# Performance work log

Measured on AMD Instinct MI355X. Metric: run time of the kernel, lower is better.

Reference implementation:

```python
import jax, jax.numpy as jnp
import numpy as np

B, P, S, D = 16, 512, 1024, 1024
H_FULL, H_LIGHT = 16, 8


def _mha(q, k, v, w_in, b_in, w_out, b_out, nh):
    # PyTorch nn.MultiheadAttention (batch_first=True), dropout=0 (eval).
    d = q.shape[-1]
    hd = d // nh
    wq, wk, wv = jnp.split(w_in, 3, axis=0)
    bq, bk, bv = jnp.split(b_in, 3, axis=0)

    def proj(x, w, b):
        return (x @ w.T + b).reshape(x.shape[0], x.shape[1], nh, hd)

    qh = proj(q, wq, bq)  # [B,Lq,H,hd]
    kh = proj(k, wk, bk)  # [B,Lk,H,hd]
    vh = proj(v, wv, bv)
    scale = 1.0 / jnp.sqrt(jnp.asarray(hd, q.dtype))
    scores = jnp.einsum('bqhd,bkhd->bhqk', qh, kh) * scale
    attn = jax.nn.softmax(scores, axis=-1)
    o = jnp.einsum('bhqk,bkhd->bqhd', attn, vh).reshape(q.shape[0], q.shape[1], d)
    out = o @ w_out.T + b_out
    return out, attn.mean(axis=1)  # avg weights over heads (torch default)


def _ln(x, g, b, eps=1e-5):
    mu = x.mean(-1, keepdims=True)
    var = ((x - mu) ** 2).mean(-1, keepdims=True)
    return (x - mu) / jnp.sqrt(var + eps) * g + b


def setup_inputs() -> dict:
    key = jax.random.key(0)
    ks = jax.random.split(key, 16)
    w = 0.02
    inp = {
        'proto': jax.random.normal(ks[0], (B, P, D), jnp.float32),
        'img_features': jax.random.normal(ks[1], (B, S, D), jnp.float32),
        'cross_w_in': jax.random.normal(ks[2], (3 * D, D), jnp.float32) * w,
        'cross_b_in': jnp.zeros((3 * D,), jnp.float32),
        'cross_w_out': jax.random.normal(ks[3], (D, D), jnp.float32) * w,
        'cross_b_out': jnp.zeros((D,), jnp.float32),
        'self_w_in': jax.random.normal(ks[4], (3 * D, D), jnp.float32) * w,
        'self_b_in': jnp.zeros((3 * D,), jnp.float32),
        'self_w_out': jax.random.normal(ks[5], (D, D), jnp.float32) * w,
        'self_b_out': jnp.zeros((D,), jnp.float32),
        'light_w_in': jax.random.normal(ks[6], (3 * D, D), jnp.float32) * w,
        'light_b_in': jnp.zeros((3 * D,), jnp.float32),
        'light_w_out': jax.random.normal(ks[7], (D, D), jnp.float32) * w,
        'light_b_out': jnp.zeros((D,), jnp.float32),
        'norm1_g': jnp.ones((D,), jnp.float32), 'norm1_b': jnp.zeros((D,), jnp.float32),
        'norm2_g': jnp.ones((D,), jnp.float32), 'norm2_b': jnp.zeros((D,), jnp.float32),
        'norm3_g': jnp.ones((D,), jnp.float32), 'norm3_b': jnp.zeros((D,), jnp.float32),
        'gate_w1': jax.random.normal(ks[8], (D, 3 * D), jnp.float32) * w,
        'gate_b1': jnp.zeros((D,), jnp.float32),
        'gate_w2': jax.random.normal(ks[9], (3, D), jnp.float32) * w,
        'gate_b2': jnp.zeros((3,), jnp.float32),
    }
    return inp


def reference(proto, img_features,
              cross_w_in, cross_b_in, cross_w_out, cross_b_out,
              self_w_in, self_b_in, self_w_out, self_b_out,
              light_w_in, light_b_in, light_w_out, light_b_out,
              norm1_g, norm1_b, norm2_g, norm2_b, norm3_g, norm3_b,
              gate_w1, gate_b1, gate_w2, gate_b2):
    cross_raw, attn_w = _mha(proto, img_features, img_features,
                             cross_w_in, cross_b_in, cross_w_out, cross_b_out, H_FULL)
    cross_out = _ln(proto + cross_raw, norm1_g, norm1_b)
    self_raw, _ = _mha(cross_out, cross_out, cross_out,
                       self_w_in, self_b_in, self_w_out, self_b_out, H_FULL)
    self_out = _ln(cross_out + self_raw, norm2_g, norm2_b)
    light_raw, _ = _mha(self_out, self_out, self_out,
                        light_w_in, light_b_in, light_w_out, light_b_out, H_LIGHT)
    light_out = _ln(self_out + light_raw, norm3_g, norm3_b)
    gate_in = jnp.concatenate([cross_out, self_out, light_out], axis=-1)  # [B,P,3D]
    h = jax.nn.gelu(gate_in @ gate_w1.T + gate_b1, approximate=False)
    gate_w = jax.nn.softmax(h @ gate_w2.T + gate_b2, axis=-1)  # [B,P,3]
    updated = (gate_w[..., 0:1] * cross_out
               + gate_w[..., 1:2] * self_out
               + gate_w[..., 2:3] * light_out)
    return updated, attn_w
```

## Files before the change

### kernel.cpp

```cpp
#include <hip/hip_runtime.h>
#include <hip/hip_bf16.h>

typedef __hip_bfloat16 bf16;
typedef __attribute__((ext_vector_type(8))) short short8;
typedef __attribute__((ext_vector_type(4))) float f32x4;

#define BD 16
#define PD 512
#define SD 1024
#define DD 1024

#define GLDS16(gp, lp)                                              \
  __builtin_amdgcn_global_load_lds(                                 \
      (const __attribute__((address_space(1))) void*)(gp),          \
      (__attribute__((address_space(3))) void*)(lp), 16, 0, 0)

__global__ __launch_bounds__(256) void f2b(const float* __restrict__ in,
                                           bf16* __restrict__ out, int n)
{
  int i = (blockIdx.x * 256 + threadIdx.x) * 4;
  if (i < n) {
    float4 v = *(const float4*)(in + i);
    out[i + 0] = __float2bfloat16(v.x);
    out[i + 1] = __float2bfloat16(v.y);
    out[i + 2] = __float2bfloat16(v.z);
    out[i + 3] = __float2bfloat16(v.w);
  }
}

__global__ __launch_bounds__(256) void gemm_nt(
    const bf16* __restrict__ A, int lda,
    const bf16* __restrict__ W, int ldw,
    const float* __restrict__ bias,
    bf16* __restrict__ C, int ldc,
    int K, int gelu)
{
  __shared__ bf16 As[3][128 * 32];
  __shared__ bf16 Bs[3][64 * 32];

  const int t = threadIdx.x;
  const int lane = t & 63, wv = t >> 6;
  const int m0 = blockIdx.y * 128;
  const int n0 = blockIdx.x * 64;
  const int rl = lane & 15, qd = lane >> 4;

  f32x4 acc[4][2];
  for (int i = 0; i < 4; i++)
    for (int j = 0; j < 2; j++)
      acc[i][j] = (f32x4){0.f, 0.f, 0.f, 0.f};

  const int scol = ((t & 3) ^ ((t >> 2) & 3)) * 8;
  const bf16* Ag = A + (size_t)(m0 + (t >> 2)) * lda + scol;
  const bf16* Wg = W + (size_t)(n0 + (t >> 2)) * ldw + scol;
  const size_t a_half = (size_t)64 * lda;
  const int lo = wv * 512;

  const int mw = (wv >> 1) * 64, nw = (wv & 1) * 32;
  const int slo = rl & 3;

  const int nt = K >> 5;

#define STAGE(buf, k0)                               \
  do {                                               \
    GLDS16(Ag + (k0), &As[buf][lo]);                 \
    GLDS16(Ag + a_half + (k0), &As[buf][2048 + lo]); \
    GLDS16(Wg + (k0), &Bs[buf][lo]);                 \
  } while (0)

  STAGE(0, 0);
  STAGE(1, 32);

  int cur = 0, pf = 2;
  for (int tt = 0; tt < nt; ++tt) {
    if (tt + 1 < nt) asm volatile("s_waitcnt vmcnt(3)" ::: "memory");
    else             asm volatile("s_waitcnt vmcnt(0)" ::: "memory");
    __builtin_amdgcn_s_barrier();
    if (tt + 2 < nt) STAGE(pf, (tt + 2) * 32);

    const bf16* Ac = As[cur];
    const bf16* Bc = Bs[cur];
    short8 a[4], b[2];
#pragma unroll
    for (int i = 0; i < 4; i++)
      a[i] = *(const short8*)&Ac[(mw + i * 16 + rl) * 32 + (qd ^ slo) * 8];
#pragma unroll
    for (int j = 0; j < 2; j++)
      b[j] = *(const short8*)&Bc[(nw + j * 16 + rl) * 32 + (qd ^ slo) * 8];
#pragma unroll
    for (int i = 0; i < 4; i++)
#pragma unroll
      for (int j = 0; j < 2; j++)
        acc[i][j] = __builtin_amdgcn_mfma_f32_16x16x32_bf16(a[i], b[j], acc[i][j], 0, 0, 0);

    cur = (cur == 2) ? 0 : cur + 1;
    pf  = (pf == 2) ? 0 : pf + 1;
  }
#undef STAGE

  for (int i = 0; i < 4; i++) {
    const int row = m0 + mw + i * 16 + qd * 4;
    for (int j = 0; j < 2; j++) {
      const int col = n0 + nw + j * 16 + rl;
      const float bv = bias[col];
      for (int r = 0; r < 4; r++) {
        float v = acc[i][j][r] + bv;
        if (gelu) v = 0.5f * v * (1.0f + erff(v * 0.70710678118654752f));
        C[(size_t)(row + r) * ldc + col] = __float2bfloat16(v);
      }
    }
  }
}

__global__ __launch_bounds__(512, 2) void gemm8p(
    const bf16* __restrict__ A, int lda,
    const bf16* __restrict__ W, int ldw,
    const float* __restrict__ bias,
    bf16* __restrict__ C, int ldc,
    int K, int gelu)
{
  __shared__ bf16 As[2][256 * 64];
  __shared__ bf16 Bs[2][256 * 64];

  const int t = threadIdx.x;
  const int lane = t & 63, wv = t >> 6;
  const int rl = lane & 15, qd = lane >> 4;
  const int m0 = blockIdx.y * 256, n0 = blockIdx.x * 256;
  const int aw = (wv >> 2) * 64;
  const int bw = (wv & 3) * 32;
  const int slo = rl & 7;

  f32x4 acc[8][4];
#pragma unroll
  for (int i = 0; i < 8; i++)
#pragma unroll
    for (int j = 0; j < 4; j++) acc[i][j] = (f32x4){0.f, 0.f, 0.f, 0.f};

  const int lr = lane >> 3;
  const int scol = ((lane & 7) ^ lr) * 8;
  const bf16* Ag = A + (size_t)(m0 + wv * 8 + lr) * lda + scol;
  const bf16* Wg = W + (size_t)(n0 + (wv >> 2) * 64 + (wv & 3) * 8 + lr) * ldw + scol;
  const int ldsw = wv * 512;

#define ST_ALO(bf_, k0_) { GLDS16(Ag + (k0_), &As[bf_][ldsw]);                     \
                           GLDS16(Ag + (size_t)128 * lda + (k0_), &As[bf_][4096 + ldsw]); }
#define ST_AHI(bf_, k0_) { GLDS16(Ag + (size_t)64 * lda + (k0_), &As[bf_][8192 + ldsw]); \
                           GLDS16(Ag + (size_t)192 * lda + (k0_), &As[bf_][12288 + ldsw]); }
#define ST_BLO(bf_, k0_) { GLDS16(Wg + (k0_), &Bs[bf_][ldsw]);                     \
                           GLDS16(Wg + (size_t)128 * ldw + (k0_), &Bs[bf_][4096 + ldsw]); }
#define ST_BHI(bf_, k0_) { GLDS16(Wg + (size_t)32 * ldw + (k0_), &Bs[bf_][8192 + ldsw]); \
                           GLDS16(Wg + (size_t)160 * ldw + (k0_), &Bs[bf_][12288 + ldsw]); }

#define PHASE(rb_, mh_, nh_, STG)                                                   \
  {                                                                                 \
    short8 a0[4][2], b0[2][2];                                                      \
    const bf16* Ab_ = &As[rb_][(size_t)((mh_) * 128 + aw) * 64];                    \
    const bf16* Bb_ = &Bs[rb_][(size_t)((nh_) * 128 + bw) * 64];                    \
    _Pragma("unroll") for (int i2 = 0; i2 < 4; i2++)                                \
      _Pragma("unroll") for (int kk = 0; kk < 2; kk++)                              \
        a0[i2][kk] = *(const short8*)&Ab_[(i2 * 16 + rl) * 64 + ((kk * 4 + qd) ^ slo) * 8]; \
    _Pragma("unroll") for (int j2 = 0; j2 < 2; j2++)                                \
      _Pragma("unroll") for (int kk = 0; kk < 2; kk++)                              \
        b0[j2][kk] = *(const short8*)&Bb_[(j2 * 16 + rl) * 64 + ((kk * 4 + qd) ^ slo) * 8]; \
    STG;                                                                            \
    asm volatile("s_waitcnt vmcnt(4)" ::: "memory");                                \
    __builtin_amdgcn_s_barrier();                                                   \
    __builtin_amdgcn_s_setprio(1);                                                  \
    _Pragma("unroll") for (int i2 = 0; i2 < 4; i2++)                                \
      _Pragma("unroll") for (int j2 = 0; j2 < 2; j2++)                              \
        _Pragma("unroll") for (int kk = 0; kk < 2; kk++)                            \
          acc[(mh_) * 4 + i2][(nh_) * 2 + j2] = __builtin_amdgcn_mfma_f32_16x16x32_bf16( \
              a0[i2][kk], b0[j2][kk], acc[(mh_) * 4 + i2][(nh_) * 2 + j2], 0, 0, 0); \
    __builtin_amdgcn_s_setprio(0);                                                  \
    __builtin_amdgcn_s_barrier();                                                   \
  }

  const int nt = K >> 6;

  ST_ALO(0, 0); ST_BLO(0, 0); ST_AHI(0, 0); ST_BHI(0, 0);
  asm volatile("s_waitcnt vmcnt(4)" ::: "memory");
  __builtin_amdgcn_s_barrier();

  for (int tt = 0; tt < nt; ++tt) {
    const int rb = tt & 1, sb = rb ^ 1;
    const int kn = (tt + 1) << 6;
    const bool st = (tt + 1) < nt;
    PHASE(rb, 0, 0, if (st) ST_ALO(sb, kn));
    PHASE(rb, 1, 0, if (st) ST_BLO(sb, kn));
    PHASE(rb, 0, 1, if (st) ST_AHI(sb, kn));
    PHASE(rb, 1, 1, if (st) ST_BHI(sb, kn));
  }
#undef PHASE
#undef ST_ALO
#undef ST_AHI
#undef ST_BLO
#undef ST_BHI

  const int mw = (wv >> 2) * 128, nw = (wv & 3) * 64;
  for (int i = 0; i < 8; i++) {
    const int row = m0 + mw + i * 16 + qd * 4;
    for (int j = 0; j < 4; j++) {
      const int col = n0 + nw + j * 16 + rl;
      const float bv = bias[col];
      for (int r = 0; r < 4; r++) {
        float v = acc[i][j][r] + bv;
        if (gelu) v = 0.5f * v * (1.0f + erff(v * 0.70710678118654752f));
        C[(size_t)(row + r) * ldc + col] = __float2bfloat16(v);
      }
    }
  }
}

__global__ void transpose_v(const bf16* __restrict__ V, int ldv, int voff,
                            bf16* __restrict__ Vt, int L, int H, int hd)
{
  __shared__ float tile[32][33];
  const int bh = blockIdx.z;
  const int b = bh / H, h = bh % H;
  const int d0 = blockIdx.x * 32, s0 = blockIdx.y * 32;
  const int tx = threadIdx.x, ty = threadIdx.y;
  tile[ty][tx] = __bfloat162float(V[(size_t)(b * L + s0 + ty) * ldv + voff + h * hd + d0 + tx]);
  __syncthreads();
  Vt[(size_t)((b * H + h) * hd + d0 + ty) * L + s0 + tx] = __float2bfloat16(tile[tx][ty]);
}

template<int HD, bool STATS>
__global__ __launch_bounds__(256) void flash_attn(
    const bf16* __restrict__ Q, int ldq, int qoff,
    const bf16* __restrict__ Km, int ldk, int koff,
    const bf16* __restrict__ Vt,
    bf16* __restrict__ O, int ldo, int ooff,
    float* __restrict__ linv_out,
    int H, int Lq, int Lk, float scale)
{
  constexpr int KK = HD / 32;
  constexpr int NO = HD / 16;
  __shared__ __align__(16) __hip_bfloat16 pl[4][2][2][16][32];

  const int lane = threadIdx.x & 63, wv = threadIdx.x >> 6;
  const int rl = lane & 15, qd = lane >> 4;
  const int b = blockIdx.z, h = blockIdx.y;
  const int q0 = blockIdx.x * 128 + wv * 32;

  short8 qf[2][KK];
  for (int mt = 0; mt < 2; ++mt)
    for (int kk = 0; kk < KK; ++kk)
      qf[mt][kk] = *(const short8*)(Q + (size_t)(b * Lq + q0 + mt * 16 + rl) * ldq
                                      + qoff + h * HD + kk * 32 + qd * 8);

  const bf16* Kb = Km + (size_t)b * Lk * ldk + koff + h * HD + qd * 8;
  const bf16* Vb = Vt + (size_t)(b * H + h) * HD * Lk + qd * 8;

  float ls[2][4];
  for (int mt = 0; mt < 2; mt++)
    for (int r = 0; r < 4; r++) ls[mt][r] = 0.f;
  f32x4 oacc[2][NO];
  for (int mt = 0; mt < 2; mt++)
    for (int ni = 0; ni < NO; ni++) oacc[mt][ni] = (f32x4){0.f, 0.f, 0.f, 0.f};

  const int nS32 = Lk / 32;
  for (int i = 0; i < nS32; i++) {
    const int s0 = i * 32;
    for (int f = 0; f < 2; f++) {
      short8 kf[KK];
#pragma unroll
      for (int kk = 0; kk < KK; kk++)
        kf[kk] = *(const short8*)(Kb + (size_t)(s0 + f * 16 + rl) * ldk + kk * 32);
#pragma unroll
      for (int mt = 0; mt < 2; mt++) {
        f32x4 sc = (f32x4){0.f, 0.f, 0.f, 0.f};
#pragma unroll
        for (int kk = 0; kk < KK; kk++)
          sc = __builtin_amdgcn_mfma_f32_16x16x32_bf16(qf[mt][kk], kf[kk], sc, 0, 0, 0);
        for (int r = 0; r < 4; r++) {
          float p = __expf(sc[r] * scale);
          ls[mt][r] += p;
          pl[wv][i & 1][mt][qd * 4 + r][f * 16 + rl] = __float2bfloat16(p);
        }
      }
    }
    asm volatile("s_waitcnt lgkmcnt(0)" ::: "memory");
    short8 vf[NO];
#pragma unroll
    for (int ni = 0; ni < NO; ni++)
      vf[ni] = *(const short8*)(Vb + (size_t)(ni * 16 + rl) * Lk + s0);
#pragma unroll
    for (int mt = 0; mt < 2; mt++) {
      short8 pa = *(const short8*)&pl[wv][i & 1][mt][rl][qd * 8];
#pragma unroll
      for (int ni = 0; ni < NO; ni++)
        oacc[mt][ni] = __builtin_amdgcn_mfma_f32_16x16x32_bf16(pa, vf[ni], oacc[mt][ni], 0, 0, 0);
    }
  }

  float rinv[2][4];
  for (int mt = 0; mt < 2; mt++)
    for (int r = 0; r < 4; r++) {
      float v = ls[mt][r];
      for (int o = 1; o < 16; o <<= 1) v += __shfl_xor(v, o);
      rinv[mt][r] = 1.0f / v;
    }

  if (STATS) {
    if (rl == 0)
      for (int mt = 0; mt < 2; mt++)
        for (int r = 0; r < 4; r++)
          linv_out[((size_t)b * H + h) * Lq + q0 + mt * 16 + qd * 4 + r] = rinv[mt][r];
  }

  for (int mt = 0; mt < 2; mt++)
    for (int ni = 0; ni < NO; ni++)
      for (int r = 0; r < 4; r++)
        O[(size_t)(b * Lq + q0 + mt * 16 + qd * 4 + r) * ldo + ooff + h * HD + ni * 16 + rl]
            = __float2bfloat16(oacc[mt][ni][r] * rinv[mt][r]);
}

template<int HD>
__global__ __launch_bounds__(256) void probs_mean(
    const bf16* __restrict__ Q, int ldq, int qoff,
    const bf16* __restrict__ Km, int ldk, int koff,
    const float* __restrict__ linv, float* __restrict__ out_att,
    int H, int Lq, int Lk, float scale)
{
  constexpr int KK = HD / 32;
  const int lane = threadIdx.x & 63, wv = threadIdx.x >> 6;
  const int rl = lane & 15, qd = lane >> 4;
  const int b = blockIdx.z;
  const int q0 = blockIdx.x * 128 + wv * 32;
  const int s0 = blockIdx.y * 32;
  const float hs = 1.0f / 16.0f;

  f32x4 am[2][2];
  for (int mt = 0; mt < 2; mt++)
    for (int f = 0; f < 2; f++) am[mt][f] = (f32x4){0.f, 0.f, 0.f, 0.f};

  const bf16* Qb  = Q  + (size_t)(b * Lq + q0) * ldq + qoff + qd * 8;
  const bf16* Kb0 = Km + (size_t)(b * Lk + s0) * ldk + koff + qd * 8;
  const float* lb = linv + (size_t)b * H * Lq + q0 + qd * 4;

  for (int h = 0; h < H; h++) {
    short8 qf[2][KK], kf[2][KK];
#pragma unroll
    for (int mt = 0; mt < 2; mt++)
#pragma unroll
      for (int kk = 0; kk < KK; kk++)
        qf[mt][kk] = *(const short8*)(Qb + (size_t)(mt * 16 + rl) * ldq + h * HD + kk * 32);
#pragma unroll
    for (int f = 0; f < 2; f++)
#pragma unroll
      for (int kk = 0; kk < KK; kk++)
        kf[f][kk] = *(const short8*)(Kb0 + (size_t)(f * 16 + rl) * ldk + h * HD + kk * 32);
    float li[2][4];
#pragma unroll
    for (int mt = 0; mt < 2; mt++)
#pragma unroll
      for (int r = 0; r < 4; r++)
        li[mt][r] = lb[(size_t)h * Lq + mt * 16 + r];
#pragma unroll
    for (int mt = 0; mt < 2; mt++)
#pragma unroll
      for (int f = 0; f < 2; f++) {
        f32x4 sc = (f32x4){0.f, 0.f, 0.f, 0.f};
#pragma unroll
        for (int kk = 0; kk < KK; kk++)
          sc = __builtin_amdgcn_mfma_f32_16x16x32_bf16(qf[mt][kk], kf[f][kk], sc, 0, 0, 0);
#pragma unroll
        for (int r = 0; r < 4; r++)
          am[mt][f][r] += __expf(sc[r] * scale) * li[mt][r];
      }
  }

#pragma unroll
  for (int mt = 0; mt < 2; mt++)
#pragma unroll
    for (int f = 0; f < 2; f++)
#pragma unroll
      for (int r = 0; r < 4; r++)
        out_att[(size_t)(b * Lq + q0 + mt * 16 + qd * 4 + r) * Lk + s0 + f * 16 + rl]
            = am[mt][f][r] * hs;
}

template<bool XF32>
__global__ __launch_bounds__(256) void add_ln(
    const void* __restrict__ Xv, int ldx, int xoff,
    const bf16* __restrict__ Y,
    const float* __restrict__ g, const float* __restrict__ bb,
    bf16* __restrict__ out, int ldo, int ooff)
{
  const int row = blockIdx.x, t = threadIdx.x;
  const bf16* yr = Y + (size_t)row * 1024;
  float v[4], s = 0.f, s2 = 0.f;
  for (int i = 0; i < 4; i++) {
    int c = t * 4 + i;
    float xv;
    if (XF32) xv = ((const float*)Xv)[(size_t)row * ldx + xoff + c];
    else      xv = __bfloat162float(((const bf16*)Xv)[(size_t)row * ldx + xoff + c]);
    v[i] = xv + __bfloat162float(yr[c]);
    s += v[i]; s2 += v[i] * v[i];
  }
  __shared__ float red[2][4];
  for (int o = 32; o >= 1; o >>= 1) { s += __shfl_down(s, o); s2 += __shfl_down(s2, o); }
  const int wv = t >> 6, lane = t & 63;
  if (lane == 0) { red[0][wv] = s; red[1][wv] = s2; }
  __syncthreads();
  s  = red[0][0] + red[0][1] + red[0][2] + red[0][3];
  s2 = red[1][0] + red[1][1] + red[1][2] + red[1][3];
  const float mean = s * (1.0f / 1024.f);
  const float var = s2 * (1.0f / 1024.f) - mean * mean;
  const float rstd = rsqrtf(var + 1e-5f);
  for (int i = 0; i < 4; i++) {
    int c = t * 4 + i;
    float o = (v[i] - mean) * rstd * g[c] + bb[c];
    out[(size_t)row * ldo + ooff + c] = __float2bfloat16(o);
  }
}

__global__ __launch_bounds__(256) void gate_kernel(
    const bf16* __restrict__ Hb, const bf16* __restrict__ G,
    const float* __restrict__ w2, const float* __restrict__ b2,
    float* __restrict__ out)
{
  const int row = blockIdx.x, t = threadIdx.x;
  const bf16* hr = Hb + (size_t)row * 1024;
  float d0 = 0.f, d1 = 0.f, d2 = 0.f;
  for (int i = 0; i < 4; i++) {
    int c = t * 4 + i;
    float hv = __bfloat162float(hr[c]);
    d0 += hv * w2[c];
    d1 += hv * w2[1024 + c];
    d2 += hv * w2[2048 + c];
  }
  __shared__ float red[3][4];
  for (int o = 32; o >= 1; o >>= 1) {
    d0 += __shfl_down(d0, o); d1 += __shfl_down(d1, o); d2 += __shfl_down(d2, o);
  }
  const int wv = t >> 6, lane = t & 63;
  if (lane == 0) { red[0][wv] = d0; red[1][wv] = d1; red[2][wv] = d2; }
  __syncthreads();
  float l0 = red[0][0] + red[0][1] + red[0][2] + red[0][3] + b2[0];
  float l1 = red[1][0] + red[1][1] + red[1][2] + red[1][3] + b2[1];
  float l2 = red[2][0] + red[2][1] + red[2][2] + red[2][3] + b2[2];
  float mm = fmaxf(l0, fmaxf(l1, l2));
  float e0 = __expf(l0 - mm), e1 = __expf(l1 - mm), e2 = __expf(l2 - mm);
  float inv = 1.f / (e0 + e1 + e2);
  float g0 = e0 * inv, g1 = e1 * inv, g2 = e2 * inv;
  const bf16* gr = G + (size_t)row * 3072;
  for (int i = 0; i < 4; i++) {
    int c = t * 4 + i;
    float o = g0 * __bfloat162float(gr[c]) + g1 * __bfloat162float(gr[1024 + c])
            + g2 * __bfloat162float(gr[2048 + c]);
    out[(size_t)row * 1024 + c] = o;
  }
}

extern "C" void kernel_launch(void* const* d_in, const int* in_sizes, int n_in,
                              void* d_out, int out_size, void* d_ws, size_t ws_size,
                              hipStream_t stream)
{
  const float* proto = (const float*)d_in[0];
  const float* img   = (const float*)d_in[1];
  const float* c_wi  = (const float*)d_in[2];
  const float* c_bi  = (const float*)d_in[3];
  const float* c_wo  = (const float*)d_in[4];
  const float* c_bo  = (const float*)d_in[5];
  const float* s_wi  = (const float*)d_in[6];
  const float* s_bi  = (const float*)d_in[7];
  const float* s_wo  = (const float*)d_in[8];
  const float* s_bo  = (const float*)d_in[9];
  const float* l_wi  = (const float*)d_in[10];
  const float* l_bi  = (const float*)d_in[11];
  const float* l_wo  = (const float*)d_in[12];
  const float* l_bo  = (const float*)d_in[13];
  const float* n1g = (const float*)d_in[14]; const float* n1b = (const float*)d_in[15];
  const float* n2g = (const float*)d_in[16]; const float* n2b = (const float*)d_in[17];
  const float* n3g = (const float*)d_in[18]; const float* n3b = (const float*)d_in[19];
  const float* gw1 = (const float*)d_in[20]; const float* gb1 = (const float*)d_in[21];
  const float* gw2 = (const float*)d_in[22]; const float* gb2 = (const float*)d_in[23];

  float* out_upd = (float*)d_out;
  float* out_att = out_upd + (size_t)BD * PD * DD;

  char* ws = (char*)d_ws;
  bf16* WB = (bf16*)ws;
  bf16* w_cwi = WB + 0;
  bf16* w_cwo = WB + 3145728;
  bf16* w_swi = WB + 4194304;
  bf16* w_swo = WB + 7340032;
  bf16* w_lwi = WB + 8388608;
  bf16* w_lwo = WB + 11534336;
  bf16* w_gw1 = WB + 12582912;

  int bc = 16;
  while (bc > 1 && 31457280ull + (size_t)bc * 16777216ull > ws_size) bc >>= 1;

  char* pool = ws + 31457280;
  bf16*  Pb    = (bf16*)pool;
  bf16*  Ib    = (bf16*)(pool + (size_t)1048576 * bc);
  bf16*  G     = (bf16*)(pool + (size_t)3145728 * bc);
  bf16*  KVb   = (bf16*)(pool + (size_t)6291456 * bc);
  bf16*  Bq    = (bf16*)(pool + (size_t)8388608 * bc);
  bf16*  Vt    = (bf16*)(pool + (size_t)11534336 * bc);
  bf16*  Qc    = (bf16*)(pool + (size_t)13631488 * bc);
  bf16*  AO    = (bf16*)(pool + (size_t)14680064 * bc);
  bf16*  OP    = (bf16*)(pool + (size_t)15728640 * bc);
  float* linvb = (float*)(pool + (size_t)15728640 * bc);

  const dim3 blk(256);
  const dim3 blk512(512);

  f2b<<<dim3(3072), blk, 0, stream>>>(c_wi, w_cwi, 3145728);
  f2b<<<dim3(1024), blk, 0, stream>>>(c_wo, w_cwo, 1048576);
  f2b<<<dim3(3072), blk, 0, stream>>>(s_wi, w_swi, 3145728);
  f2b<<<dim3(1024), blk, 0, stream>>>(s_wo, w_swo, 1048576);
  f2b<<<dim3(3072), blk, 0, stream>>>(l_wi, w_lwi, 3145728);
  f2b<<<dim3(1024), blk, 0, stream>>>(l_wo, w_lwo, 1048576);
  f2b<<<dim3(3072), blk, 0, stream>>>(gw1, w_gw1, 3145728);

  for (int b0 = 0; b0 < BD; b0 += bc) {
    const float* proto_c = proto + (size_t)b0 * PD * DD;
    const float* img_c   = img + (size_t)b0 * SD * DD;
    float* out_upd_c = out_upd + (size_t)b0 * PD * DD;
    float* out_att_c = out_att + (size_t)b0 * PD * SD;
    const int MP = bc * PD;
    const int MS = bc * SD;

    f2b<<<dim3(MP), blk, 0, stream>>>(proto_c, Pb, MP * DD);
    f2b<<<dim3(MS), blk, 0, stream>>>(img_c, Ib, MS * DD);

    gemm_nt<<<dim3(16, MP / 128), blk, 0, stream>>>(Pb, 1024, w_cwi, 1024, c_bi,
                                                    Qc, 1024, 1024, 0);
    gemm8p<<<dim3(8, MS / 256), blk512, 0, stream>>>(
        Ib, 1024, w_cwi + (size_t)1024 * 1024, 1024, c_bi + 1024, KVb, 2048, 1024, 0);
    transpose_v<<<dim3(2, 32, bc * 16), dim3(32, 32), 0, stream>>>(KVb, 2048, 1024, Vt, 1024, 16, 64);
    flash_attn<64, true><<<dim3(4, 16, bc), blk, 0, stream>>>(
        Qc, 1024, 0, KVb, 2048, 0, Vt, AO, 1024, 0, linvb, 16, PD, SD, 0.125f);
    probs_mean<64><<<dim3(4, SD / 32, bc), blk, 0, stream>>>(
        Qc, 1024, 0, KVb, 2048, 0, linvb, out_att_c, 16, PD, SD, 0.125f);
    gemm_nt<<<dim3(16, MP / 128), blk, 0, stream>>>(AO, 1024, w_cwo, 1024, c_bo, OP, 1024, 1024, 0);
    add_ln<true><<<dim3(MP), blk, 0, stream>>>(proto_c, 1024, 0, OP, n1g, n1b, G, 3072, 0);

    gemm8p<<<dim3(12, MP / 256), blk512, 0, stream>>>(
        G, 3072, w_swi, 1024, s_bi, Bq, 3072, 1024, 0);
    transpose_v<<<dim3(2, 16, bc * 16), dim3(32, 32), 0, stream>>>(Bq, 3072, 2048, Vt, 512, 16, 64);
    flash_attn<64, false><<<dim3(4, 16, bc), blk, 0, stream>>>(
        Bq, 3072, 0, Bq, 3072, 1024, Vt, AO, 1024, 0, nullptr, 16, PD, PD, 0.125f);
    gemm_nt<<<dim3(16, MP / 128), blk, 0, stream>>>(AO, 1024, w_swo, 1024, s_bo, OP, 1024, 1024, 0);
    add_ln<false><<<dim3(MP), blk, 0, stream>>>(G, 3072, 0, OP, n2g, n2b, G, 3072, 1024);

    gemm8p<<<dim3(12, MP / 256), blk512, 0, stream>>>(
        G + 1024, 3072, w_lwi, 1024, l_bi, Bq, 3072, 1024, 0);
    transpose_v<<<dim3(4, 16, bc * 8), dim3(32, 32), 0, stream>>>(Bq, 3072, 2048, Vt, 512, 8, 128);
    flash_attn<128, false><<<dim3(4, 8, bc), blk, 0, stream>>>(
        Bq, 3072, 0, Bq, 3072, 1024, Vt, AO, 1024, 0, nullptr, 8, PD, PD,
        0.08838834764831845f);
    gemm_nt<<<dim3(16, MP / 128), blk, 0, stream>>>(AO, 1024, w_lwo, 1024, l_bo, OP, 1024, 1024, 0);
    add_ln<false><<<dim3(MP), blk, 0, stream>>>(G, 3072, 1024, OP, n3g, n3b, G, 3072, 2048);

    gemm_nt<<<dim3(16, MP / 128), blk, 0, stream>>>(G, 3072, w_gw1, 3072, gb1, Qc, 1024, 3072, 1);
    gate_kernel<<<dim3(MP), blk, 0, stream>>>(Qc, G, gw2, gb2, out_upd_c);
  }
}
```

Before: 1.344 ms.

## Halve flash-attention query tile per wave, swizzle P in LDS, prefetch V

Each wave now handles 16 query rows instead of 32, doubling the grid in x to keep coverage the same. This raises parallelism and cuts register use, but halves K/V reuse per load. The P scratch tile in LDS is XOR-swizzled to reduce bank conflicts on the transposed readback. V fragment loads are issued before the QK step so their latency overlaps the score computation.

Result: slower. 1.525 ms (+13.4%).

```diff
diff --git a/kernel.cpp b/kernel.cpp
--- a/kernel.cpp
+++ b/kernel.cpp
@@ -234,84 +234,81 @@
 {
   constexpr int KK = HD / 32;
   constexpr int NO = HD / 16;
-  __shared__ __align__(16) __hip_bfloat16 pl[4][2][2][16][32];
+  __shared__ __align__(16) __hip_bfloat16 pl[4][2][16][32];
 
   const int lane = threadIdx.x & 63, wv = threadIdx.x >> 6;
   const int rl = lane & 15, qd = lane >> 4;
   const int b = blockIdx.z, h = blockIdx.y;
-  const int q0 = blockIdx.x * 128 + wv * 32;
-
-  short8 qf[2][KK];
-  for (int mt = 0; mt < 2; ++mt)
-    for (int kk = 0; kk < KK; ++kk)
-      qf[mt][kk] = *(const short8*)(Q + (size_t)(b * Lq + q0 + mt * 16 + rl) * ldq
-                                      + qoff + h * HD + kk * 32 + qd * 8);
+  const int q0 = blockIdx.x * 64 + wv * 16;
+
+  short8 qf[KK];
+#pragma unroll
+  for (int kk = 0; kk < KK; ++kk)
+    qf[kk] = *(const short8*)(Q + (size_t)(b * Lq + q0 + rl) * ldq
+                                + qoff + h * HD + kk * 32 + qd * 8);
 
   const bf16* Kb = Km + (size_t)b * Lk * ldk + koff + h * HD + qd * 8;
   const bf16* Vb = Vt + (size_t)(b * H + h) * HD * Lk + qd * 8;
 
-  float ls[2][4];
-  for (int mt = 0; mt < 2; mt++)
-    for (int r = 0; r < 4; r++) ls[mt][r] = 0.f;
-  f32x4 oacc[2][NO];
-  for (int mt = 0; mt < 2; mt++)
-    for (int ni = 0; ni < NO; ni++) oacc[mt][ni] = (f32x4){0.f, 0.f, 0.f, 0.f};
-
+  float ls[4] = {0.f, 0.f, 0.f, 0.f};
+  f32x4 oacc[NO];
+#pragma unroll
+  for (int ni = 0; ni < NO; ni++) oacc[ni] = (f32x4){0.f, 0.f, 0.f, 0.f};
+
+  const int swr = (rl >> 2) & 3;
   const int nS32 = Lk / 32;
   for (int i = 0; i < nS32; i++) {
     const int s0 = i * 32;
+    short8 vf[NO];
+#pragma unroll
+    for (int ni = 0; ni < NO; ni++)
+      vf[ni] = *(const short8*)(Vb + (size_t)(ni * 16 + rl) * Lk + s0);
+#pragma unroll
     for (int f = 0; f < 2; f++) {
       short8 kf[KK];
 #pragma unroll
       for (int kk = 0; kk < KK; kk++)
         kf[kk] = *(const short8*)(Kb + (size_t)(s0 + f * 16 + rl) * ldk + kk * 32);
-#pragma unroll
-      for (int mt = 0; mt < 2; mt++) {
-        f32x4 sc = (f32x4){0.f, 0.f, 0.f, 0.f};
-#pragma unroll
-        for (int kk = 0; kk < KK; kk++)
-          sc = __builtin_amdgcn_mfma_f32_16x16x32_bf16(qf[mt][kk], kf[kk], sc, 0, 0, 0);
-        for (int r = 0; r < 4; r++) {
-          float p = __expf(sc[r] * scale);
-          ls[mt][r] += p;
-          pl[wv][i & 1][mt][qd * 4 + r][f * 16 + rl] = __float2bfloat16(p);
-        }
+      f32x4 sc = (f32x4){0.f, 0.f, 0.f, 0.f};
+#pragma unroll
+      for (int kk = 0; kk < KK; kk++)
+        sc = __builtin_amdgcn_mfma_f32_16x16x32_bf16(qf[kk], kf[kk], sc, 0, 0, 0);
+#pragma unroll
+      for (int r = 0; r < 4; r++) {
+        float p = __expf(sc[r] * scale);
+        ls[r] += p;
+        pl[wv][i & 1][qd * 4 + r][(((f * 2 + (rl >> 3)) ^ qd) * 8) + (rl & 7)]
+            = __float2bfloat16(p);
       }
     }
     asm volatile("s_waitcnt lgkmcnt(0)" ::: "memory");
-    short8 vf[NO];
+    short8 pa = *(const short8*)&pl[wv][i & 1][rl][(qd ^ swr) * 8];
 #pragma unroll
     for (int ni = 0; ni < NO; ni++)
-      vf[ni] = *(const short8*)(Vb + (size_t)(ni * 16 + rl) * Lk + s0);
-#pragma unroll
-    for (int mt = 0; mt < 2; mt++) {
-      short8 pa = *(const short8*)&pl[wv][i & 1][mt][rl][qd * 8];
-#pragma unroll
-      for (int ni = 0; ni < NO; ni++)
-        oacc[mt][ni] = __builtin_amdgcn_mfma_f32_16x16x32_bf16(pa, vf[ni], oacc[mt][ni], 0, 0, 0);
-    }
-  }
-
-  float rinv[2][4];
-  for (int mt = 0; mt < 2; mt++)
-    for (int r = 0; r < 4; r++) {
-      float v = ls[mt][r];
-      for (int o = 1; o < 16; o <<= 1) v += __shfl_xor(v, o);
-      rinv[mt][r] = 1.0f / v;
-    }
+      oacc[ni] = __builtin_amdgcn_mfma_f32_16x16x32_bf16(pa, vf[ni], oacc[ni], 0, 0, 0);
+  }
+
+  float rinv[4];
+#pragma unroll
+  for (int r = 0; r < 4; r++) {
+    float v = ls[r];
+    for (int o = 1; o < 16; o <<= 1) v += __shfl_xor(v, o);
+    rinv[r] = 1.0f / v;
+  }
 
   if (STATS) {
     if (rl == 0)
-      for (int mt = 0; mt < 2; mt++)
-        for (int r = 0; r < 4; r++)
-          linv_out[((size_t)b * H + h) * Lq + q0 + mt * 16 + qd * 4 + r] = rinv[mt][r];
-  }
-
-  for (int mt = 0; mt < 2; mt++)
-    for (int ni = 0; ni < NO; ni++)
+#pragma unroll
       for (int r = 0; r < 4; r++)
-        O[(size_t)(b * Lq + q0 + mt * 16 + qd * 4 + r) * ldo + ooff + h * HD + ni * 16 + rl]
-            = __float2bfloat16(oacc[mt][ni][r] * rinv[mt][r]);
+        linv_out[((size_t)b * H + h) * Lq + q0 + qd * 4 + r] = rinv[r];
+  }
+
+#pragma unroll
+  for (int ni = 0; ni < NO; ni++)
+#pragma unroll
+    for (int r = 0; r < 4; r++)
+      O[(size_t)(b * Lq + q0 + qd * 4 + r) * ldo + ooff + h * HD + ni * 16 + rl]
+          = __float2bfloat16(oacc[ni][r] * rinv[r]);
 }
 
 template<int HD>
@@ -531,7 +528,7 @@
     gemm8p<<<dim3(8, MS / 256), blk512, 0, stream>>>(
         Ib, 1024, w_cwi + (size_t)1024 * 1024, 1024, c_bi + 1024, KVb, 2048, 1024, 0);
     transpose_v<<<dim3(2, 32, bc * 16), dim3(32, 32), 0, stream>>>(KVb, 2048, 1024, Vt, 1024, 16, 64);
-    flash_attn<64, true><<<dim3(4, 16, bc), blk, 0, stream>>>(
+    flash_attn<64, true><<<dim3(8, 16, bc), blk, 0, stream>>>(
         Qc, 1024, 0, KVb, 2048, 0, Vt, AO, 1024, 0, linvb, 16, PD, SD, 0.125f);
     probs_mean<64><<<dim3(4, SD / 32, bc), blk, 0, stream>>>(
         Qc, 1024, 0, KVb, 2048, 0, linvb, out_att_c, 16, PD, SD, 0.125f);
@@ -541,7 +538,7 @@
     gemm8p<<<dim3(12, MP / 256), blk512, 0, stream>>>(
         G, 3072, w_swi, 1024, s_bi, Bq, 3072, 1024, 0);
     transpose_v<<<dim3(2, 16, bc * 16), dim3(32, 32), 0, stream>>>(Bq, 3072, 2048, Vt, 512, 16, 64);
-    flash_attn<64, false><<<dim3(4, 16, bc), blk, 0, stream>>>(
+    flash_attn<64, false><<<dim3(8, 16, bc), blk, 0, stream>>>(
         Bq, 3072, 0, Bq, 3072, 1024, Vt, AO, 1024, 0, nullptr, 16, PD, PD, 0.125f);
     gemm_nt<<<dim3(16, MP / 128), blk, 0, stream>>>(AO, 1024, w_swo, 1024, s_bo, OP, 1024, 1024, 0);
     add_ln<false><<<dim3(MP), blk, 0, stream>>>(G, 3072, 0, OP, n2g, n2b, G, 3072, 1024);
@@ -549,7 +546,7 @@
     gemm8p<<<dim3(12, MP / 256), blk512, 0, stream>>>(
         G + 1024, 3072, w_lwi, 1024, l_bi, Bq, 3072, 1024, 0);
     transpose_v<<<dim3(4, 16, bc * 8), dim3(32, 32), 0, stream>>>(Bq, 3072, 2048, Vt, 512, 8, 128);
-    flash_attn<128, false><<<dim3(4, 8, bc), blk, 0, stream>>>(
+    flash_attn<128, false><<<dim3(8, 8, bc), blk, 0, stream>>>(
         Bq, 3072, 0, Bq, 3072, 1024, Vt, AO, 1024, 0, nullptr, 8, PD, PD,
         0.08838834764831845f);
     gemm_nt<<<dim3(16, MP / 128), blk, 0, stream>>>(AO, 1024, w_lwo, 1024, l_bo, OP, 1024, 1024, 0);
```

## Double-buffer K/V register fragments in flash attention to prefetch the next tile

Applied to the files above, without the earlier changes.

Restructures the flash attention inner loop into a manually unrolled two-step pipeline that loads the next 32-key block of V (and K when head dim is 64) into a second register set while the current block is computed. For larger head dims only V is prefetched, to limit register pressure. The aim is to hide global-memory latency behind the MFMA and exp work. The cost is more VGPRs, which may reduce occupancy, and the loop now assumes an even number of key blocks.

New measurement: 1.354 ms. About the same (+0.7%).

```diff
diff --git a/kernel.cpp b/kernel.cpp
--- a/kernel.cpp
+++ b/kernel.cpp
@@ -234,6 +234,7 @@
 {
   constexpr int KK = HD / 32;
   constexpr int NO = HD / 16;
+  constexpr bool PK = (HD == 64);
   __shared__ __align__(16) __hip_bfloat16 pl[4][2][2][16][32];
 
   const int lane = threadIdx.x & 63, wv = threadIdx.x >> 6;
@@ -258,39 +259,60 @@
     for (int ni = 0; ni < NO; ni++) oacc[mt][ni] = (f32x4){0.f, 0.f, 0.f, 0.f};
 
   const int nS32 = Lk / 32;
-  for (int i = 0; i < nS32; i++) {
-    const int s0 = i * 32;
-    for (int f = 0; f < 2; f++) {
-      short8 kf[KK];
-#pragma unroll
-      for (int kk = 0; kk < KK; kk++)
-        kf[kk] = *(const short8*)(Kb + (size_t)(s0 + f * 16 + rl) * ldk + kk * 32);
-#pragma unroll
-      for (int mt = 0; mt < 2; mt++) {
-        f32x4 sc = (f32x4){0.f, 0.f, 0.f, 0.f};
-#pragma unroll
-        for (int kk = 0; kk < KK; kk++)
-          sc = __builtin_amdgcn_mfma_f32_16x16x32_bf16(qf[mt][kk], kf[kk], sc, 0, 0, 0);
-        for (int r = 0; r < 4; r++) {
-          float p = __expf(sc[r] * scale);
-          ls[mt][r] += p;
-          pl[wv][i & 1][mt][qd * 4 + r][f * 16 + rl] = __float2bfloat16(p);
-        }
-      }
+
+  short8 kA[2][KK], kB[2][KK], vA[NO], vB[NO];
+
+#define LOADK(dst, s0_) {                                                        \
+    _Pragma("unroll") for (int f = 0; f < 2; f++)                                \
+      _Pragma("unroll") for (int kk = 0; kk < KK; kk++)                          \
+        dst[f][kk] = *(const short8*)(Kb + (size_t)((s0_) + f * 16 + rl) * ldk + kk * 32); }
+#define LOADV(dst, s0_) {                                                        \
+    _Pragma("unroll") for (int ni = 0; ni < NO; ni++)                            \
+      dst[ni] = *(const short8*)(Vb + (size_t)(ni * 16 + rl) * Lk + (s0_)); }
+
+#define FSTEP(ib, KC, VC, KN, VN) {                                              \
+    const int s0_ = (ib) * 32;                                                   \
+    if ((ib) + 1 < nS32) {                                                       \
+      if constexpr (PK) LOADK(KN, s0_ + 32);                                     \
+      LOADV(VN, s0_ + 32);                                                       \
+    }                                                                            \
+    if constexpr (!PK) LOADK(KC, s0_);                                           \
+    _Pragma("unroll") for (int f = 0; f < 2; f++)                                \
+      _Pragma("unroll") for (int mt = 0; mt < 2; mt++) {                         \
+        f32x4 sc = (f32x4){0.f, 0.f, 0.f, 0.f};                                  \
+        _Pragma("unroll") for (int kk = 0; kk < KK; kk++)                        \
+          sc = __builtin_amdgcn_mfma_f32_16x16x32_bf16(qf[mt][kk], KC[f][kk], sc, 0, 0, 0); \
+        _Pragma("unroll") for (int r = 0; r < 4; r++) {                          \
+          float p = __expf(sc[r] * scale);                                       \
+          ls[mt][r] += p;                                                        \
+          pl[wv][(ib) & 1][mt][qd * 4 + r][f * 16 + rl] = __float2bfloat16(p);   \
+        }                                                                        \
+      }                                                                          \
+    asm volatile("s_waitcnt lgkmcnt(0)" ::: "memory");                           \
+    _Pragma("unroll") for (int mt = 0; mt < 2; mt++) {                           \
+      short8 pa = *(const short8*)&pl[wv][(ib) & 1][mt][rl][qd * 8];             \
+      _Pragma("unroll") for (int ni = 0; ni < NO; ni++)                          \
+        oacc[mt][ni] = __builtin_amdgcn_mfma_f32_16x16x32_bf16(pa, VC[ni], oacc[mt][ni], 0, 0, 0); \
+    }                                                                            \
+  }
+
+  if constexpr (PK) LOADK(kA, 0);
+  LOADV(vA, 0);
+
+  if constexpr (PK) {
+    for (int i = 0; i < nS32; i += 2) {
+      FSTEP(i, kA, vA, kB, vB);
+      FSTEP(i + 1, kB, vB, kA, vA);
     }
-    asm volatile("s_waitcnt lgkmcnt(0)" ::: "memory");
-    short8 vf[NO];
-#pragma unroll
-    for (int ni = 0; ni < NO; ni++)
-      vf[ni] = *(const short8*)(Vb + (size_t)(ni * 16 + rl) * Lk + s0);
-#pragma unroll
-    for (int mt = 0; mt < 2; mt++) {
-      short8 pa = *(const short8*)&pl[wv][i & 1][mt][rl][qd * 8];
-#pragma unroll
-      for (int ni = 0; ni < NO; ni++)
-        oacc[mt][ni] = __builtin_amdgcn_mfma_f32_16x16x32_bf16(pa, vf[ni], oacc[mt][ni], 0, 0, 0);
+  } else {
+    for (int i = 0; i < nS32; i += 2) {
+      FSTEP(i, kA, vA, kA, vB);
+      FSTEP(i + 1, kA, vB, kA, vA);
     }
   }
+#undef FSTEP
+#undef LOADK
+#undef LOADV
 
   float rinv[2][4];
   for (int mt = 0; mt < 2; mt++)
```
